# Kernel tuning notes

Hardware: AMD Instinct MI355X
Metric: run time of the kernel (lower is better)

## Reference

```python
import jax, jax.numpy as jnp
import numpy as np

B, T_DEC, T_ENC, H = 4, 512, 1024, 128


def setup_inputs() -> dict:
    key = jax.random.key(0)
    k1, k2, k3, k4, k5 = jax.random.split(key, 5)
    s = 1.0 / np.sqrt(H)
    return {
        "decoder_outputs": jax.random.normal(k1, (B, T_DEC, H), dtype=jnp.float32),
        "encoder_outputs": jax.random.normal(k2, (B, T_ENC, H), dtype=jnp.float32),
        "W_w": jax.random.normal(k3, (H, H), dtype=jnp.float32) * s,
        "W_b": jax.random.normal(k4, (H,), dtype=jnp.float32) * s,
        "V_w": jax.random.normal(k5, (H,), dtype=jnp.float32) * s,
        "V_b": jnp.zeros((), dtype=jnp.float32),
    }


def reference(decoder_outputs, encoder_outputs, W_w, W_b, V_w, V_b):
    # dec_transformed = W(dec): (B, T_dec, H)
    dec_t = jnp.einsum("bdh,kh->bdk", decoder_outputs, W_w) + W_b
    # broadcast add -> (B, T_dec, T_enc, H), tanh, project with V -> (B, T_dec, T_enc)
    score = jnp.tanh(dec_t[:, :, None, :] + encoder_outputs[:, None, :, :])
    score = jnp.einsum("bdeh,h->bde", score, V_w) + V_b
    attn = jax.nn.softmax(score, axis=-1)  # over T_enc
    # context = attn @ enc : (B, T_dec, H)
    context = jnp.einsum("bde,beh->bdh", attn, encoder_outputs)
    return context
```

## Files before the change

kernel.cpp:

```cpp
#include <hip/hip_runtime.h>
#include <math.h>

#define B_    4
#define TDEC  512
#define TENC  1024
#define H_    128
#define DT    4

typedef float f2 __attribute__((ext_vector_type(2)));

__device__ _Float16 g_ebp[(size_t)B_ * 16 * TENC * 8];
__device__ _Float16 g_ench[(size_t)B_ * TENC * H_];
__device__ float g_eav[(size_t)B_ * 128 * 32 * 20];
__device__ float g_sv[1];

struct EAVP { float4 v4; f2 hd[8]; };
union F4 { float4 v; float f[4]; };
union H8 { float4 v; _Float16 h[8]; };
union H4 { ushort4 u4; _Float16 h[4]; };
union H2 { unsigned int u; _Float16 h[2]; };

static __device__ __forceinline__ f2 bc(float x) { f2 r = {x, x}; return r; }

__global__ __launch_bounds__(256) void prep_kernel(const float* __restrict__ enc,
                                                   const float* __restrict__ dec,
                                                   const float* __restrict__ Ww,
                                                   const float* __restrict__ Wb,
                                                   const float* __restrict__ Vw) {
    const int z = blockIdx.z;
    const int tx = threadIdx.x, ty = threadIdx.y;
    if (z < B_) {
        __shared__ float tile[32][33];
        const int e0 = blockIdx.x * 32, h0 = blockIdx.y * 32, b = z;
        const float* ep = enc + (size_t)b * TENC * H_;
        #pragma unroll
        for (int j = 0; j < 32; j += 8) {
            const float v = ep[(size_t)(e0 + ty + j) * H_ + h0 + tx];
            tile[ty + j][tx] = v;
            g_ench[(size_t)b * TENC * H_ + (size_t)(e0 + ty + j) * H_ + h0 + tx]
                = (_Float16)v;
        }
        __syncthreads();
        const int g = (h0 >> 2) + ty, e = e0 + tx;
        const int gp = g >> 1, hs = g & 1;
        H4 o;
        o.h[0] = (_Float16)fminf(__expf(2.f * tile[tx][4 * ty + 0]), 60000.f);
        o.h[1] = (_Float16)fminf(__expf(2.f * tile[tx][4 * ty + 1]), 60000.f);
        o.h[2] = (_Float16)fminf(__expf(2.f * tile[tx][4 * ty + 2]), 60000.f);
        o.h[3] = (_Float16)fminf(__expf(2.f * tile[tx][4 * ty + 3]), 60000.f);
        *(ushort4*)&g_ebp[((((size_t)b * 16 + gp) * TENC) + e) * 8 + hs * 4] = o.u4;
    } else {
        __shared__ float ds[16][H_];
        const int t = ty * 32 + tx;
        const int blk = blockIdx.y * 32 + blockIdx.x;
        const int R0 = blk * 16;
        #pragma unroll
        for (int i = 0; i < 8; ++i) {
            const int f = t + 256 * i;
            ds[f >> 7][f & 127] = dec[(size_t)R0 * H_ + f];
        }
        __syncthreads();
        const int k = t & 127, dd = t >> 7;
        const float* wr = Ww + (size_t)k * H_;
        float s[8];
        #pragma unroll
        for (int j = 0; j < 8; ++j) s[j] = 0.f;
        for (int h = 0; h < H_; h += 4) {
            const float4 w4 = *(const float4*)(wr + h);
            #pragma unroll
            for (int j = 0; j < 8; ++j) {
                const float4 d4 = *(const float4*)&ds[dd + 2 * j][h];
                s[j] = fmaf(w4.x, d4.x, s[j]);
                s[j] = fmaf(w4.y, d4.y, s[j]);
                s[j] = fmaf(w4.z, d4.z, s[j]);
                s[j] = fmaf(w4.w, d4.w, s[j]);
            }
        }
        const float wb = Wb[k], vw = Vw[k];
        const int g = k >> 2, jj = k & 3;
        #pragma unroll
        for (int j = 0; j < 8; ++j) {
            const int rl = dd + 2 * j;
            const int R = R0 + rl;
            const float ea = __expf(2.f * (s[j] + wb));
            g_eav[((size_t)(R >> 2) * 32 + g) * 20 + 4 + jj * 4 + (R & 3)] = ea;
        }
        if (dd == 0) {
            #pragma unroll
            for (int r = 0; r < 4; ++r)
                g_eav[((size_t)((R0 >> 2) + r) * 32 + g) * 20 + jj] = vw;
        }
        if (blk == 0) {
            __shared__ float svp[2];
            if (t < 128) {
                float x = vw;
                #pragma unroll
                for (int off = 32; off; off >>= 1) x += __shfl_xor(x, off);
                if ((t & 63) == 0) svp[t >> 6] = x;
            }
            __syncthreads();
            if (t == 0) g_sv[0] = svp[0] + svp[1];
        }
    }
}

__device__ __forceinline__ f2 term4p(f2 p0, f2 p1, f2 p2, f2 p3,
                                     const float4 v4, f2 acc) {
    const f2 q01 = p0 * p1, q23 = p2 * p3;
    const f2 a   = __builtin_elementwise_fma(bc(v4.y), p0, bc(v4.x) * p1);
    const f2 bq  = __builtin_elementwise_fma(bc(v4.w), p2, bc(v4.z) * p3);
    const f2 num = __builtin_elementwise_fma(bq, q01, a * q23);
    const f2 den = q01 * q23;
    f2 r;
    r.x = __builtin_amdgcn_rcpf(den.x);
    r.y = __builtin_amdgcn_rcpf(den.y);
    return __builtin_elementwise_fma(num, r, acc);
}

#define DALLP(S, t0, t1, t2, t3) do {                                          \
    const f2 one2 = {1.f, 1.f};                                                \
    f2 pA0 = __builtin_elementwise_fma(S.hd[0], bc(t0), one2);                 \
    f2 pB0 = __builtin_elementwise_fma(S.hd[1], bc(t0), one2);                 \
    f2 pA1 = __builtin_elementwise_fma(S.hd[2], bc(t1), one2);                 \
    f2 pB1 = __builtin_elementwise_fma(S.hd[3], bc(t1), one2);                 \
    f2 pA2 = __builtin_elementwise_fma(S.hd[4], bc(t2), one2);                 \
    f2 pB2 = __builtin_elementwise_fma(S.hd[5], bc(t2), one2);                 \
    f2 pA3 = __builtin_elementwise_fma(S.hd[6], bc(t3), one2);                 \
    f2 pB3 = __builtin_elementwise_fma(S.hd[7], bc(t3), one2);                 \
    acc01 = term4p(pA0, pA1, pA2, pA3, S.v4, acc01);                           \
    acc23 = term4p(pB0, pB1, pB2, pB3, S.v4, acc23);                           \
} while (0)

__global__ __launch_bounds__(1024, 8) void fused_kernel(float* __restrict__ out) {
    __shared__ float sc[DT][TENC];
    __shared__ f2 part[16][DT][64];
    __shared__ float wsum[16][DT];
    __shared__ float rsum[DT];

    const int t = threadIdx.x;
    const int bid = blockIdx.x;
    const int rt = (bid & 7) * 64 + (bid >> 3);
    const int b = rt >> 7;
    const int R0 = rt * DT;
    const EAVP* epk = (const EAVP*)g_eav + (size_t)rt * 32;
    const _Float16* teb = g_ebp + (size_t)b * 16 * TENC * 8 + t * 8;
    const float sv = g_sv[0];

    f2 acc01 = {0.f, 0.f}, acc23 = {0.f, 0.f};

    for (int gp = 0; gp < 16; ++gp) {
        H8 r;
        r.v = *(const float4*)(teb + (size_t)gp * (TENC * 8));
        const float t0 = (float)r.h[0], t1 = (float)r.h[1];
        const float t2 = (float)r.h[2], t3 = (float)r.h[3];
        const float t4 = (float)r.h[4], t5 = (float)r.h[5];
        const float t6 = (float)r.h[6], t7 = (float)r.h[7];
        const EAVP A  = epk[2 * gp];
        const EAVP Bv = epk[2 * gp + 1];
        DALLP(A, t0, t1, t2, t3);
        DALLP(Bv, t4, t5, t6, t7);
    }

    const float q0 = __expf(fmaf(-2.f, acc01.x, sv));
    const float q1 = __expf(fmaf(-2.f, acc01.y, sv));
    const float q2 = __expf(fmaf(-2.f, acc23.x, sv));
    const float q3 = __expf(fmaf(-2.f, acc23.y, sv));
    sc[0][t] = q0; sc[1][t] = q1; sc[2][t] = q2; sc[3][t] = q3;

    float s0 = q0, s1 = q1, s2 = q2, s3 = q3;
    #pragma unroll
    for (int off = 32; off; off >>= 1) {
        s0 += __shfl_xor(s0, off);
        s1 += __shfl_xor(s1, off);
        s2 += __shfl_xor(s2, off);
        s3 += __shfl_xor(s3, off);
    }
    {
        const int w = t >> 6, lane = t & 63;
        if (lane == 0) { wsum[w][0] = s0; wsum[w][1] = s1; wsum[w][2] = s2; wsum[w][3] = s3; }
    }
    __syncthreads();
    if (t < 64) {
        float x = wsum[t >> 2][t & 3];
        #pragma unroll
        for (int off = 4; off < 64; off <<= 1) x += __shfl_xor(x, off);
        if (t < 4) rsum[t] = x;
    }

    {
        const int q = t >> 6, h2 = t & 63;
        const _Float16* eb = g_ench + (size_t)b * TENC * H_ + 2 * h2;
        f2 a0 = {0.f, 0.f}, a1 = {0.f, 0.f}, a2 = {0.f, 0.f}, a3 = {0.f, 0.f};
        const int e0 = q * 64;
        for (int e = e0; e < e0 + 64; e += 4) {
            F4 u0, u1, u2, u3;
            u0.v = *(const float4*)&sc[0][e];
            u1.v = *(const float4*)&sc[1][e];
            u2.v = *(const float4*)&sc[2][e];
            u3.v = *(const float4*)&sc[3][e];
            #pragma unroll
            for (int j = 0; j < 4; ++j) {
                H2 hv; hv.u = *(const unsigned int*)(eb + (size_t)(e + j) * H_);
                f2 ev; ev.x = (float)hv.h[0]; ev.y = (float)hv.h[1];
                a0 = __builtin_elementwise_fma(bc(u0.f[j]), ev, a0);
                a1 = __builtin_elementwise_fma(bc(u1.f[j]), ev, a1);
                a2 = __builtin_elementwise_fma(bc(u2.f[j]), ev, a2);
                a3 = __builtin_elementwise_fma(bc(u3.f[j]), ev, a3);
            }
        }
        part[q][0][h2] = a0; part[q][1][h2] = a1;
        part[q][2][h2] = a2; part[q][3][h2] = a3;
    }
    __syncthreads();

    if (t < 256) {
        const int d = t >> 6, h2 = t & 63;
        f2 s = {0.f, 0.f};
        #pragma unroll
        for (int q = 0; q < 16; ++q) s += part[q][d][h2];
        const float rinv = __builtin_amdgcn_rcpf(rsum[d]);
        s *= bc(rinv);
        *(f2*)(out + (size_t)(R0 + d) * H_ + 2 * h2) = s;
    }
}

extern "C" void kernel_launch(void* const* d_in, const int* in_sizes, int n_in,
                              void* d_out, int out_size, void* d_ws, size_t ws_size,
                              hipStream_t stream) {
    const float* dec = (const float*)d_in[0];
    const float* enc = (const float*)d_in[1];
    const float* Ww  = (const float*)d_in[2];
    const float* Wb  = (const float*)d_in[3];
    const float* Vw  = (const float*)d_in[4];
    float* out = (float*)d_out;

    prep_kernel<<<dim3(TENC / 32, H_ / 32, B_ + 1), dim3(32, 8), 0, stream>>>(
        enc, dec, Ww, Wb, Vw);
    fused_kernel<<<dim3(B_ * 128), dim3(1024), 0, stream>>>(out);
}
```

Baseline: 43.17 us.

## Double-buffer tanh-table loads via LDS DMA and transpose fp16 encoder for context

```diff
diff --git a/kernel.cpp b/kernel.cpp
--- a/kernel.cpp
+++ b/kernel.cpp
@@ -10,7 +10,7 @@
 typedef float f2 __attribute__((ext_vector_type(2)));
 
 __device__ _Float16 g_ebp[(size_t)B_ * 16 * TENC * 8];
-__device__ _Float16 g_ench[(size_t)B_ * TENC * H_];
+__device__ _Float16 g_encht[(size_t)B_ * H_ * TENC];
 __device__ float g_eav[(size_t)B_ * 128 * 32 * 20];
 __device__ float g_sv[1];
 
@@ -18,7 +18,6 @@
 union F4 { float4 v; float f[4]; };
 union H8 { float4 v; _Float16 h[8]; };
 union H4 { ushort4 u4; _Float16 h[4]; };
-union H2 { unsigned int u; _Float16 h[2]; };
 
 static __device__ __forceinline__ f2 bc(float x) { f2 r = {x, x}; return r; }
 
@@ -34,12 +33,8 @@
         const int e0 = blockIdx.x * 32, h0 = blockIdx.y * 32, b = z;
         const float* ep = enc + (size_t)b * TENC * H_;
         #pragma unroll
-        for (int j = 0; j < 32; j += 8) {
-            const float v = ep[(size_t)(e0 + ty + j) * H_ + h0 + tx];
-            tile[ty + j][tx] = v;
-            g_ench[(size_t)b * TENC * H_ + (size_t)(e0 + ty + j) * H_ + h0 + tx]
-                = (_Float16)v;
-        }
+        for (int j = 0; j < 32; j += 8)
+            tile[ty + j][tx] = ep[(size_t)(e0 + ty + j) * H_ + h0 + tx];
         __syncthreads();
         const int g = (h0 >> 2) + ty, e = e0 + tx;
         const int gp = g >> 1, hs = g & 1;
@@ -49,6 +44,10 @@
         o.h[2] = (_Float16)fminf(__expf(2.f * tile[tx][4 * ty + 2]), 60000.f);
         o.h[3] = (_Float16)fminf(__expf(2.f * tile[tx][4 * ty + 3]), 60000.f);
         *(ushort4*)&g_ebp[((((size_t)b * 16 + gp) * TENC) + e) * 8 + hs * 4] = o.u4;
+        #pragma unroll
+        for (int k = 0; k < 4; ++k)
+            g_encht[((size_t)b * H_ + (h0 + 4 * ty + k)) * TENC + e]
+                = (_Float16)tile[tx][4 * ty + k];
     } else {
         __shared__ float ds[16][H_];
         const int t = ty * 32 + tx;
@@ -131,26 +130,42 @@
     acc23 = term4p(pB0, pB1, pB2, pB3, S.v4, acc23);                           \
 } while (0)
 
+#define DMA16(ldst, gsrc)                                                      \
+    __builtin_amdgcn_global_load_lds(                                          \
+        (__attribute__((address_space(1))) void*)(gsrc),                       \
+        (__attribute__((address_space(3))) void*)(ldst), 16, 0, 0)
+
 __global__ __launch_bounds__(1024, 8) void fused_kernel(float* __restrict__ out) {
-    __shared__ float sc[DT][TENC];
-    __shared__ f2 part[16][DT][64];
-    __shared__ float wsum[16][DT];
-    __shared__ float rsum[DT];
+    __shared__ __align__(16) char shbuf[49424];
+    float* sc    = (float*)shbuf;
+    float* alias = (float*)(shbuf + 16384);
+    float* wsum  = (float*)(shbuf + 49152);
+    float* rsum  = (float*)(shbuf + 49408);
 
     const int t = threadIdx.x;
+    const int w = t >> 6, lane = t & 63;
     const int bid = blockIdx.x;
     const int rt = (bid & 7) * 64 + (bid >> 3);
     const int b = rt >> 7;
     const int R0 = rt * DT;
     const EAVP* epk = (const EAVP*)g_eav + (size_t)rt * 32;
-    const _Float16* teb = g_ebp + (size_t)b * 16 * TENC * 8 + t * 8;
+    const _Float16* gte = g_ebp + (size_t)b * 16 * TENC * 8 + (size_t)t * 8;
     const float sv = g_sv[0];
 
+    float* tbw = alias + w * 512;
+
+    DMA16(tbw + 0,   gte + 0 * (TENC * 8));
+    DMA16(tbw + 256, gte + 1 * (TENC * 8));
+
     f2 acc01 = {0.f, 0.f}, acc23 = {0.f, 0.f};
 
+    #pragma unroll
     for (int gp = 0; gp < 16; ++gp) {
+        if (gp < 15) { asm volatile("s_waitcnt vmcnt(1)" ::: "memory"); }
+        else         { asm volatile("s_waitcnt vmcnt(0)" ::: "memory"); }
+        __builtin_amdgcn_sched_barrier(4);
         H8 r;
-        r.v = *(const float4*)(teb + (size_t)gp * (TENC * 8));
+        r.v = *(const float4*)(tbw + (gp & 1) * 256 + lane * 4);
         const float t0 = (float)r.h[0], t1 = (float)r.h[1];
         const float t2 = (float)r.h[2], t3 = (float)r.h[3];
         const float t4 = (float)r.h[4], t5 = (float)r.h[5];
@@ -159,13 +174,17 @@
         const EAVP Bv = epk[2 * gp + 1];
         DALLP(A, t0, t1, t2, t3);
         DALLP(Bv, t4, t5, t6, t7);
+        __builtin_amdgcn_sched_barrier(4);
+        if (gp < 14)
+            DMA16(tbw + (gp & 1) * 256, gte + (size_t)(gp + 2) * (TENC * 8));
     }
 
     const float q0 = __expf(fmaf(-2.f, acc01.x, sv));
     const float q1 = __expf(fmaf(-2.f, acc01.y, sv));
     const float q2 = __expf(fmaf(-2.f, acc23.x, sv));
     const float q3 = __expf(fmaf(-2.f, acc23.y, sv));
-    sc[0][t] = q0; sc[1][t] = q1; sc[2][t] = q2; sc[3][t] = q3;
+    sc[0 * TENC + t] = q0; sc[1 * TENC + t] = q1;
+    sc[2 * TENC + t] = q2; sc[3 * TENC + t] = q3;
 
     float s0 = q0, s1 = q1, s2 = q2, s3 = q3;
     #pragma unroll
@@ -175,49 +194,68 @@
         s2 += __shfl_xor(s2, off);
         s3 += __shfl_xor(s3, off);
     }
-    {
-        const int w = t >> 6, lane = t & 63;
-        if (lane == 0) { wsum[w][0] = s0; wsum[w][1] = s1; wsum[w][2] = s2; wsum[w][3] = s3; }
+    if (lane == 0) {
+        wsum[w * 4 + 0] = s0; wsum[w * 4 + 1] = s1;
+        wsum[w * 4 + 2] = s2; wsum[w * 4 + 3] = s3;
     }
     __syncthreads();
     if (t < 64) {
-        float x = wsum[t >> 2][t & 3];
+        float x = wsum[(t >> 2) * 4 + (t & 3)];
         #pragma unroll
         for (int off = 4; off < 64; off <<= 1) x += __shfl_xor(x, off);
         if (t < 4) rsum[t] = x;
     }
 
     {
-        const int q = t >> 6, h2 = t & 63;
-        const _Float16* eb = g_ench + (size_t)b * TENC * H_ + 2 * h2;
+        const int q = w, h2 = lane;
+        const _Float16* ebA = g_encht + ((size_t)b * H_ + 2 * h2) * TENC + q * 64;
+        const _Float16* ebB = ebA + TENC;
         f2 a0 = {0.f, 0.f}, a1 = {0.f, 0.f}, a2 = {0.f, 0.f}, a3 = {0.f, 0.f};
-        const int e0 = q * 64;
-        for (int e = e0; e < e0 + 64; e += 4) {
-            F4 u0, u1, u2, u3;
-            u0.v = *(const float4*)&sc[0][e];
-            u1.v = *(const float4*)&sc[1][e];
-            u2.v = *(const float4*)&sc[2][e];
-            u3.v = *(const float4*)&sc[3][e];
+        #pragma unroll
+        for (int ee = 0; ee < 64; ee += 8) {
+            H8 ra, rb;
+            ra.v = *(const float4*)(ebA + ee);
+            rb.v = *(const float4*)(ebB + ee);
+            F4 u0a, u0b, u1a, u1b, u2a, u2b, u3a, u3b;
+            u0a.v = *(const float4*)&sc[0 * TENC + q * 64 + ee];
+            u0b.v = *(const float4*)&sc[0 * TENC + q * 64 + ee + 4];
+            u1a.v = *(const float4*)&sc[1 * TENC + q * 64 + ee];
+            u1b.v = *(const float4*)&sc[1 * TENC + q * 64 + ee + 4];
+            u2a.v = *(const float4*)&sc[2 * TENC + q * 64 + ee];
+            u2b.v = *(const float4*)&sc[2 * TENC + q * 64 + ee + 4];
+            u3a.v = *(const float4*)&sc[3 * TENC + q * 64 + ee];
+            u3b.v = *(const float4*)&sc[3 * TENC + q * 64 + ee + 4];
             #pragma unroll
             for (int j = 0; j < 4; ++j) {
-                H2 hv; hv.u = *(const unsigned int*)(eb + (size_t)(e + j) * H_);
-                f2 ev; ev.x = (float)hv.h[0]; ev.y = (float)hv.h[1];
-                a0 = __builtin_elementwise_fma(bc(u0.f[j]), ev, a0);
-                a1 = __builtin_elementwise_fma(bc(u1.f[j]), ev, a1);
-                a2 = __builtin_elementwise_fma(bc(u2.f[j]), ev, a2);
-                a3 = __builtin_elementwise_fma(bc(u3.f[j]), ev, a3);
-            }
-        }
-        part[q][0][h2] = a0; part[q][1][h2] = a1;
-        part[q][2][h2] = a2; part[q][3][h2] = a3;
+                f2 ev; ev.x = (float)ra.h[j]; ev.y = (float)rb.h[j];
+                a0 = __builtin_elementwise_fma(bc(u0a.f[j]), ev, a0);
+                a1 = __builtin_elementwise_fma(bc(u1a.f[j]), ev, a1);
+                a2 = __builtin_elementwise_fma(bc(u2a.f[j]), ev, a2);
+                a3 = __builtin_elementwise_fma(bc(u3a.f[j]), ev, a3);
+            }
+            #pragma unroll
+            for (int j = 0; j < 4; ++j) {
+                f2 ev; ev.x = (float)ra.h[4 + j]; ev.y = (float)rb.h[4 + j];
+                a0 = __builtin_elementwise_fma(bc(u0b.f[j]), ev, a0);
+                a1 = __builtin_elementwise_fma(bc(u1b.f[j]), ev, a1);
+                a2 = __builtin_elementwise_fma(bc(u2b.f[j]), ev, a2);
+                a3 = __builtin_elementwise_fma(bc(u3b.f[j]), ev, a3);
+            }
+        }
+        f2* part = (f2*)alias;
+        part[q * 256 + 0 * 64 + h2] = a0;
+        part[q * 256 + 1 * 64 + h2] = a1;
+        part[q * 256 + 2 * 64 + h2] = a2;
+        part[q * 256 + 3 * 64 + h2] = a3;
     }
     __syncthreads();
 
     if (t < 256) {
         const int d = t >> 6, h2 = t & 63;
+        const f2* part = (const f2*)alias;
         f2 s = {0.f, 0.f};
         #pragma unroll
-        for (int q = 0; q < 16; ++q) s += part[q][d][h2];
+        for (int q = 0; q < 16; ++q) s += part[q * 256 + d * 64 + h2];
         const float rinv = __builtin_amdgcn_rcpf(rsum[d]);
         s *= bc(rinv);
         *(f2*)(out + (size_t)(R0 + d) * H_ + 2 * h2) = s;
```

Result: slower. 80.84 us (+87.2%).

## Stage per-row coefficients in LDS and double-buffer encoder loads with inline asm

Applied to the files above, without the earlier changes.

```diff
diff --git a/kernel.cpp b/kernel.cpp
--- a/kernel.cpp
+++ b/kernel.cpp
@@ -8,6 +8,7 @@
 #define DT    4
 
 typedef float f2 __attribute__((ext_vector_type(2)));
+typedef float vf4 __attribute__((ext_vector_type(4)));
 
 __device__ _Float16 g_ebp[(size_t)B_ * 16 * TENC * 8];
 __device__ _Float16 g_ench[(size_t)B_ * TENC * H_];
@@ -16,7 +17,7 @@
 
 struct EAVP { float4 v4; f2 hd[8]; };
 union F4 { float4 v; float f[4]; };
-union H8 { float4 v; _Float16 h[8]; };
+union H8 { vf4 v; _Float16 h[8]; };
 union H4 { ushort4 u4; _Float16 h[4]; };
 union H2 { unsigned int u; _Float16 h[2]; };
 
@@ -131,36 +132,57 @@
     acc23 = term4p(pB0, pB1, pB2, pB3, S.v4, acc23);                           \
 } while (0)
 
-__global__ __launch_bounds__(1024, 8) void fused_kernel(float* __restrict__ out) {
+#define GLOAD(dst, ptr) \
+    asm volatile("global_load_dwordx4 %0, %1, off" : "=&v"(dst) : "v"(ptr))
+
+#define P1ITER(GP, RCUR, CNT) do {                                             \
+    const EAVP A  = *(const EAVP*)(evbuf + (2 * (GP) + 0) * 20);               \
+    const EAVP Bv = *(const EAVP*)(evbuf + (2 * (GP) + 1) * 20);               \
+    asm volatile("s_waitcnt vmcnt(" #CNT ")" ::: "memory");                    \
+    __builtin_amdgcn_sched_barrier(0);                                         \
+    H8 r; r.v = RCUR;                                                          \
+    const float t0 = (float)r.h[0], t1 = (float)r.h[1];                        \
+    const float t2 = (float)r.h[2], t3 = (float)r.h[3];                        \
+    const float t4 = (float)r.h[4], t5 = (float)r.h[5];                        \
+    const float t6 = (float)r.h[6], t7 = (float)r.h[7];                        \
+    if ((GP) + 2 < 16) { GLOAD(RCUR, pcur); pcur += TENC * 8; }                \
+    DALLP(A,  t0, t1, t2, t3);                                                 \
+    DALLP(Bv, t4, t5, t6, t7);                                                 \
+} while (0)
+
+__global__ __launch_bounds__(1024) void fused_kernel(float* __restrict__ out) {
     __shared__ float sc[DT][TENC];
     __shared__ f2 part[16][DT][64];
     __shared__ float wsum[16][DT];
     __shared__ float rsum[DT];
+    __shared__ __align__(16) float evbuf[640];
 
     const int t = threadIdx.x;
     const int bid = blockIdx.x;
     const int rt = (bid & 7) * 64 + (bid >> 3);
     const int b = rt >> 7;
     const int R0 = rt * DT;
-    const EAVP* epk = (const EAVP*)g_eav + (size_t)rt * 32;
-    const _Float16* teb = g_ebp + (size_t)b * 16 * TENC * 8 + t * 8;
+    const _Float16* gte = g_ebp + (size_t)b * 16 * TENC * 8 + (size_t)t * 8;
+
+    if (t < 640) evbuf[t] = g_eav[(size_t)rt * 640 + t];
+    __syncthreads();
+
+    f2 acc01 = {0.f, 0.f}, acc23 = {0.f, 0.f};
+    vf4 rA, rB;
+    GLOAD(rA, gte + 0 * (TENC * 8));
+    GLOAD(rB, gte + 1 * (TENC * 8));
+    const _Float16* pcur = gte + 2 * (TENC * 8);
+
+    P1ITER(0,  rA, 1);  P1ITER(1,  rB, 1);
+    P1ITER(2,  rA, 1);  P1ITER(3,  rB, 1);
+    P1ITER(4,  rA, 1);  P1ITER(5,  rB, 1);
+    P1ITER(6,  rA, 1);  P1ITER(7,  rB, 1);
+    P1ITER(8,  rA, 1);  P1ITER(9,  rB, 1);
+    P1ITER(10, rA, 1);  P1ITER(11, rB, 1);
+    P1ITER(12, rA, 1);  P1ITER(13, rB, 1);
+    P1ITER(14, rA, 1);  P1ITER(15, rB, 0);
+
     const float sv = g_sv[0];
-
-    f2 acc01 = {0.f, 0.f}, acc23 = {0.f, 0.f};
-
-    for (int gp = 0; gp < 16; ++gp) {
-        H8 r;
-        r.v = *(const float4*)(teb + (size_t)gp * (TENC * 8));
-        const float t0 = (float)r.h[0], t1 = (float)r.h[1];
-        const float t2 = (float)r.h[2], t3 = (float)r.h[3];
-        const float t4 = (float)r.h[4], t5 = (float)r.h[5];
-        const float t6 = (float)r.h[6], t7 = (float)r.h[7];
-        const EAVP A  = epk[2 * gp];
-        const EAVP Bv = epk[2 * gp + 1];
-        DALLP(A, t0, t1, t2, t3);
-        DALLP(Bv, t4, t5, t6, t7);
-    }
-
     const float q0 = __expf(fmaf(-2.f, acc01.x, sv));
     const float q1 = __expf(fmaf(-2.f, acc01.y, sv));
     const float q2 = __expf(fmaf(-2.f, acc23.x, sv));
```

New measurement: 46.84 us. 1.09x slower.

## Compute context with fp16 MFMA over swizzled LDS attention weights

Applied to the files above, without the earlier changes.

```diff
diff --git a/kernel.cpp b/kernel.cpp
--- a/kernel.cpp
+++ b/kernel.cpp
@@ -8,17 +8,17 @@
 #define DT    4
 
 typedef float f2 __attribute__((ext_vector_type(2)));
+typedef float f32x4v __attribute__((ext_vector_type(4)));
+typedef _Float16 h8v __attribute__((ext_vector_type(8)));
 
 __device__ _Float16 g_ebp[(size_t)B_ * 16 * TENC * 8];
-__device__ _Float16 g_ench[(size_t)B_ * TENC * H_];
+__device__ _Float16 g_encB[(size_t)B_ * 8 * 32 * 64 * 8];
 __device__ float g_eav[(size_t)B_ * 128 * 32 * 20];
 __device__ float g_sv[1];
 
 struct EAVP { float4 v4; f2 hd[8]; };
-union F4 { float4 v; float f[4]; };
-union H8 { float4 v; _Float16 h[8]; };
-union H4 { ushort4 u4; _Float16 h[4]; };
-union H2 { unsigned int u; _Float16 h[2]; };
+union H8u { float4 v; _Float16 h[8]; h8v hv; };
+union H4u { ushort4 u4; _Float16 h[4]; };
 
 static __device__ __forceinline__ f2 bc(float x) { f2 r = {x, x}; return r; }
 
@@ -34,21 +34,25 @@
         const int e0 = blockIdx.x * 32, h0 = blockIdx.y * 32, b = z;
         const float* ep = enc + (size_t)b * TENC * H_;
         #pragma unroll
-        for (int j = 0; j < 32; j += 8) {
-            const float v = ep[(size_t)(e0 + ty + j) * H_ + h0 + tx];
-            tile[ty + j][tx] = v;
-            g_ench[(size_t)b * TENC * H_ + (size_t)(e0 + ty + j) * H_ + h0 + tx]
-                = (_Float16)v;
-        }
+        for (int j = 0; j < 32; j += 8)
+            tile[ty + j][tx] = ep[(size_t)(e0 + ty + j) * H_ + h0 + tx];
         __syncthreads();
         const int g = (h0 >> 2) + ty, e = e0 + tx;
         const int gp = g >> 1, hs = g & 1;
-        H4 o;
+        H4u o;
         o.h[0] = (_Float16)fminf(__expf(2.f * tile[tx][4 * ty + 0]), 60000.f);
         o.h[1] = (_Float16)fminf(__expf(2.f * tile[tx][4 * ty + 1]), 60000.f);
         o.h[2] = (_Float16)fminf(__expf(2.f * tile[tx][4 * ty + 2]), 60000.f);
         o.h[3] = (_Float16)fminf(__expf(2.f * tile[tx][4 * ty + 3]), 60000.f);
         *(ushort4*)&g_ebp[((((size_t)b * 16 + gp) * TENC) + e) * 8 + hs * 4] = o.u4;
+        const int kk = e >> 5, lg = (e >> 3) & 3, jj = e & 7;
+        #pragma unroll
+        for (int k = 0; k < 4; ++k) {
+            const int h = h0 + 4 * ty + k;
+            const int n = h >> 4, hl = h & 15;
+            g_encB[((((size_t)b * 8 + n) * 32 + kk) * 64 + (lg * 16 + hl)) * 8 + jj]
+                = (_Float16)tile[tx][4 * ty + k];
+        }
     } else {
         __shared__ float ds[16][H_];
         const int t = ty * 32 + tx;
@@ -132,12 +136,13 @@
 } while (0)
 
 __global__ __launch_bounds__(1024, 8) void fused_kernel(float* __restrict__ out) {
-    __shared__ float sc[DT][TENC];
-    __shared__ f2 part[16][DT][64];
-    __shared__ float wsum[16][DT];
-    __shared__ float rsum[DT];
+    __shared__ __align__(16) _Float16 sc_h[16 * TENC];
+    __shared__ float wred[16][4];
+    __shared__ float rmax4[4], rsum4[4];
+    __shared__ __align__(16) float cx[8][16][4];
 
     const int t = threadIdx.x;
+    const int w = t >> 6, lane = t & 63;
     const int bid = blockIdx.x;
     const int rt = (bid & 7) * 64 + (bid >> 3);
     const int b = rt >> 7;
@@ -146,10 +151,15 @@
     const _Float16* teb = g_ebp + (size_t)b * 16 * TENC * 8 + t * 8;
     const float sv = g_sv[0];
 
+    {
+        int* z = (int*)sc_h + 2048;
+        #pragma unroll
+        for (int i = 0; i < 6; ++i) z[t + 1024 * i] = 0;
+    }
+
     f2 acc01 = {0.f, 0.f}, acc23 = {0.f, 0.f};
-
     for (int gp = 0; gp < 16; ++gp) {
-        H8 r;
+        H8u r;
         r.v = *(const float4*)(teb + (size_t)gp * (TENC * 8));
         const float t0 = (float)r.h[0], t1 = (float)r.h[1];
         const float t2 = (float)r.h[2], t3 = (float)r.h[3];
@@ -161,66 +171,81 @@
         DALLP(Bv, t4, t5, t6, t7);
     }
 
-    const float q0 = __expf(fmaf(-2.f, acc01.x, sv));
-    const float q1 = __expf(fmaf(-2.f, acc01.y, sv));
-    const float q2 = __expf(fmaf(-2.f, acc23.x, sv));
-    const float q3 = __expf(fmaf(-2.f, acc23.y, sv));
-    sc[0][t] = q0; sc[1][t] = q1; sc[2][t] = q2; sc[3][t] = q3;
-
-    float s0 = q0, s1 = q1, s2 = q2, s3 = q3;
-    #pragma unroll
-    for (int off = 32; off; off >>= 1) {
-        s0 += __shfl_xor(s0, off);
-        s1 += __shfl_xor(s1, off);
-        s2 += __shfl_xor(s2, off);
-        s3 += __shfl_xor(s3, off);
-    }
-    {
-        const int w = t >> 6, lane = t & 63;
-        if (lane == 0) { wsum[w][0] = s0; wsum[w][1] = s1; wsum[w][2] = s2; wsum[w][3] = s3; }
+    const float s0 = fmaf(-2.f, acc01.x, sv);
+    const float s1 = fmaf(-2.f, acc01.y, sv);
+    const float s2 = fmaf(-2.f, acc23.x, sv);
+    const float s3 = fmaf(-2.f, acc23.y, sv);
+    {
+        float m0 = s0, m1 = s1, m2 = s2, m3 = s3;
+        #pragma unroll
+        for (int off = 32; off; off >>= 1) {
+            m0 = fmaxf(m0, __shfl_xor(m0, off));
+            m1 = fmaxf(m1, __shfl_xor(m1, off));
+            m2 = fmaxf(m2, __shfl_xor(m2, off));
+            m3 = fmaxf(m3, __shfl_xor(m3, off));
+        }
+        if (lane == 0) { wred[w][0] = m0; wred[w][1] = m1; wred[w][2] = m2; wred[w][3] = m3; }
     }
     __syncthreads();
     if (t < 64) {
-        float x = wsum[t >> 2][t & 3];
+        float x = wred[t >> 2][t & 3];
+        #pragma unroll
+        for (int off = 4; off < 64; off <<= 1) x = fmaxf(x, __shfl_xor(x, off));
+        if (t < 4) rmax4[t] = x;
+    }
+    __syncthreads();
+    {
+        const _Float16 h0 = (_Float16)__expf(s0 - rmax4[0]);
+        const _Float16 h1 = (_Float16)__expf(s1 - rmax4[1]);
+        const _Float16 h2 = (_Float16)__expf(s2 - rmax4[2]);
+        const _Float16 h3 = (_Float16)__expf(s3 - rmax4[3]);
+        *(_Float16*)((char*)sc_h + ((0 * 2048 + t * 2) ^ 0))  = h0;
+        *(_Float16*)((char*)sc_h + ((1 * 2048 + t * 2) ^ 16)) = h1;
+        *(_Float16*)((char*)sc_h + ((2 * 2048 + t * 2) ^ 32)) = h2;
+        *(_Float16*)((char*)sc_h + ((3 * 2048 + t * 2) ^ 48)) = h3;
+        float f0 = (float)h0, f1 = (float)h1, f2s = (float)h2, f3 = (float)h3;
+        #pragma unroll
+        for (int off = 32; off; off >>= 1) {
+            f0 += __shfl_xor(f0, off);
+            f1 += __shfl_xor(f1, off);
+            f2s += __shfl_xor(f2s, off);
+            f3 += __shfl_xor(f3, off);
+        }
+        if (lane == 0) { wred[w][0] = f0; wred[w][1] = f1; wred[w][2] = f2s; wred[w][3] = f3; }
+    }
+    __syncthreads();
+    if (t < 64) {
+        float x = wred[t >> 2][t & 3];
         #pragma unroll
         for (int off = 4; off < 64; off <<= 1) x += __shfl_xor(x, off);
-        if (t < 4) rsum[t] = x;
-    }
-
-    {
-        const int q = t >> 6, h2 = t & 63;
-        const _Float16* eb = g_ench + (size_t)b * TENC * H_ + 2 * h2;
-        f2 a0 = {0.f, 0.f}, a1 = {0.f, 0.f}, a2 = {0.f, 0.f}, a3 = {0.f, 0.f};
-        const int e0 = q * 64;
-        for (int e = e0; e < e0 + 64; e += 4) {
-            F4 u0, u1, u2, u3;
-            u0.v = *(const float4*)&sc[0][e];
-            u1.v = *(const float4*)&sc[1][e];
-            u2.v = *(const float4*)&sc[2][e];
-            u3.v = *(const float4*)&sc[3][e];
-            #pragma unroll
-            for (int j = 0; j < 4; ++j) {
-                H2 hv; hv.u = *(const unsigned int*)(eb + (size_t)(e + j) * H_);
-                f2 ev; ev.x = (float)hv.h[0]; ev.y = (float)hv.h[1];
-                a0 = __builtin_elementwise_fma(bc(u0.f[j]), ev, a0);
-                a1 = __builtin_elementwise_fma(bc(u1.f[j]), ev, a1);
-                a2 = __builtin_elementwise_fma(bc(u2.f[j]), ev, a2);
-                a3 = __builtin_elementwise_fma(bc(u3.f[j]), ev, a3);
-            }
-        }
-        part[q][0][h2] = a0; part[q][1][h2] = a1;
-        part[q][2][h2] = a2; part[q][3][h2] = a3;
-    }
-    __syncthreads();
-
-    if (t < 256) {
-        const int d = t >> 6, h2 = t & 63;
-        f2 s = {0.f, 0.f};
-        #pragma unroll
-        for (int q = 0; q < 16; ++q) s += part[q][d][h2];
-        const float rinv = __builtin_amdgcn_rcpf(rsum[d]);
-        s *= bc(rinv);
-        *(f2*)(out + (size_t)(R0 + d) * H_ + 2 * h2) = s;
+        if (t < 4) rsum4[t] = x;
+    }
+
+    {
+        const int n = w & 7, kh = w >> 3;
+        const int row = lane & 15, lg = lane >> 4;
+        f32x4v acc = {0.f, 0.f, 0.f, 0.f};
+        const int ab = row * 2048 + kh * 1024 + lg * 16;
+        const int swz = (row & 7) << 4;
+        const char* bptr = (const char*)g_encB
+            + ((((size_t)b * 8 + n) * 32 + kh * 16) * 64 + lane) * 16;
+        #pragma unroll
+        for (int ks = 0; ks < 16; ++ks) {
+            H8u au, bu;
+            au.v = *(const float4*)((const char*)sc_h + ((ab + ks * 64) ^ swz));
+            bu.v = *(const float4*)(bptr + ks * 1024);
+            acc = __builtin_amdgcn_mfma_f32_16x16x32_f16(au.hv, bu.hv, acc, 0, 0, 0);
+        }
+        if (w >= 8 && lane < 16) *(f32x4v*)&cx[n][lane][0] = acc;
+        __syncthreads();
+        if (w < 8 && lane < 16) {
+            const f32x4v c2 = *(const f32x4v*)&cx[n][lane][0];
+            float* op = out + (size_t)R0 * H_ + n * 16 + lane;
+            op[0 * H_] = (acc.x + c2.x) * __builtin_amdgcn_rcpf(rsum4[0]);
+            op[1 * H_] = (acc.y + c2.y) * __builtin_amdgcn_rcpf(rsum4[1]);
+            op[2 * H_] = (acc.z + c2.z) * __builtin_amdgcn_rcpf(rsum4[2]);
+            op[3 * H_] = (acc.w + c2.w) * __builtin_amdgcn_rcpf(rsum4[3]);
+        }
     }
 }
 
```

Measured after the change: 41.63 us. 3.6% less time.
